# Kernel tuning notes

Hardware: AMD Instinct MI355X
Metric: run time of the kernel (lower is better)

Reference implementation:

```python
import jax, jax.numpy as jnp
import numpy as np

LATENT = 128   # latent_size
FDIM = 32      # feature_dim per plane
FSIZE = 512    # feature_size -> grid is (FSIZE+1)^2
HID = 256      # hidden_dim
N = 500000     # number of query points
IN_DIM = 3
G = FSIZE + 1
SDF_IN = 3 * FDIM + LATENT + IN_DIM  # 227


def setup_inputs() -> dict:
    key = jax.random.key(0)
    ks = jax.random.split(key, 6)
    x = jax.random.normal(ks[0], (N, LATENT + IN_DIM), jnp.float32)
    # 3 tri-planes, each [FDIM, G, G], init randn*0.01 as in FeaturePlanes
    P = jax.random.normal(ks[1], (3, FDIM, G, G), jnp.float32) * 0.01

    def lin(k, fan_in, fan_out):
        s = 1.0 / np.sqrt(fan_in)
        kw, kb = jax.random.split(k)
        W = jax.random.uniform(kw, (fan_in, fan_out), jnp.float32, -s, s)
        b = jax.random.uniform(kb, (fan_out,), jnp.float32, -s, s)
        return W, b

    W0, b0 = lin(ks[2], SDF_IN, HID)
    W1, b1 = lin(ks[3], HID, HID)
    W2, b2 = lin(ks[4], HID, 1)
    return dict(x=x, P=P, W0=W0, b0=b0, W1=W1, b1=b1, W2=W2, b2=b2)


def _sample_plane(plane, uv):
    """Bilinear grid_sample, align_corners=True, padding_mode='border'.
    plane: [C, G, G]; uv: [Npts, 2] with uv[:,0]->width(x), uv[:,1]->height(y).
    Returns [Npts, C]."""
    g = jnp.clip((uv + 1.0) * 0.5 * (G - 1), 0.0, G - 1)  # unnormalize + border clamp
    gx, gy = g[:, 0], g[:, 1]
    x0f, y0f = jnp.floor(gx), jnp.floor(gy)
    x0 = x0f.astype(jnp.int32)
    y0 = y0f.astype(jnp.int32)
    x1 = jnp.minimum(x0 + 1, G - 1)
    y1 = jnp.minimum(y0 + 1, G - 1)
    wx = gx - x0f
    wy = gy - y0f
    v00 = plane[:, y0, x0]  # [C, Npts]
    v01 = plane[:, y0, x1]
    v10 = plane[:, y1, x0]
    v11 = plane[:, y1, x1]
    top = v00 * (1.0 - wx) + v01 * wx
    bot = v10 * (1.0 - wx) + v11 * wx
    return (top * (1.0 - wy) + bot * wy).T  # [Npts, C]


def reference(x, P, W0, b0, W1, b1, W2, b2):
    in_latents = x[:, :LATENT]
    in_x = x[:, -3:]
    coords = jax.lax.stop_gradient(in_x)  # matches .detach() before grid_sample
    # dimension pairs (0,1), (0,2), (1,2) -> one bilinear lookup each, vmapped
    uv = jnp.stack([coords[:, [0, 1]], coords[:, [0, 2]], coords[:, [1, 2]]])  # [3,N,2]
    feats = jax.vmap(_sample_plane)(P, uv)              # [3, N, FDIM]
    feats = jnp.transpose(feats, (1, 0, 2)).reshape(x.shape[0], 3 * FDIM)
    net_in = jnp.concatenate([in_latents, in_x, feats], axis=-1)  # [N, 227]
    h = jax.nn.relu(net_in @ W0 + b0)
    h = jax.nn.relu(h @ W1 + b1)
    out = (h @ W2 + b2).squeeze(-1)  # [N]
    return out
```

## Files before the change

kernel.cpp:

```cpp
#include <hip/hip_runtime.h>
#include <stdint.h>

#define XDIM 131
#define GSZ 513
#define TROWS 64
#define SC_OFF 32768

typedef __attribute__((ext_vector_type(8))) short bf16x8;
typedef __attribute__((ext_vector_type(4))) float f32x4;
typedef unsigned int uint32;

__device__ __forceinline__ unsigned short f2bf(float f) {
  uint32 u = __float_as_uint(f);
  u += 0x7fffu + ((u >> 16) & 1u);
  return (unsigned short)(u >> 16);
}
__device__ __forceinline__ float bf2f(unsigned short s) {
  return __uint_as_float(((uint32)s) << 16);
}
__device__ __forceinline__ uint32 pk2bf(float a, float b) {
  return (uint32)f2bf(a) | ((uint32)f2bf(b) << 16);
}
__device__ __forceinline__ int slot16(int r) { return (r * 16) ^ (((r >> 3) & 1) << 5); }

__global__ void prep_pt(const float* __restrict__ P, unsigned short* __restrict__ Pt) {
  int i = blockIdx.x * 256 + threadIdx.x;
  const int CELLS = 3 * GSZ * GSZ;
  if (i >= CELLS) return;
  int pl = i / (GSZ * GSZ);
  int yx = i - pl * (GSZ * GSZ);
  const float* src = P + (size_t)pl * 32 * GSZ * GSZ + yx;
  const size_t GG = (size_t)GSZ * GSZ;
  uint4* dst = (uint4*)(Pt + (size_t)i * 32);
#pragma unroll
  for (int w = 0; w < 4; ++w) {
    uint4 t;
    t.x = pk2bf(src[(w * 8 + 0) * GG], src[(w * 8 + 1) * GG]);
    t.y = pk2bf(src[(w * 8 + 2) * GG], src[(w * 8 + 3) * GG]);
    t.z = pk2bf(src[(w * 8 + 4) * GG], src[(w * 8 + 5) * GG]);
    t.w = pk2bf(src[(w * 8 + 6) * GG], src[(w * 8 + 7) * GG]);
    dst[w] = t;
  }
}

__global__ void prep_w(const float* __restrict__ W0, const float* __restrict__ W1,
                       unsigned short* __restrict__ W0g, unsigned short* __restrict__ W1g) {
  int i = blockIdx.x * 256 + threadIdx.x;
  int sel = i >> 13;
  int t = i & 8191;
  int kb = t >> 10;
  int g  = (t >> 8) & 3;
  int n  = t & 255;
  float vv[8];
#pragma unroll
  for (int j = 0; j < 8; ++j) {
    int k = kb * 32 + g * 8 + j;
    float val;
    if (sel == 0) {
      int src = (k < 131) ? k : ((k >= 136 && k < 232) ? k - 5 : -1);
      val = (src >= 0) ? W0[src * 256 + n] : 0.f;
    } else {
      val = W1[k * 256 + n];
    }
    vv[j] = val;
  }
  uint4 o;
  o.x = pk2bf(vv[0], vv[1]);
  o.y = pk2bf(vv[2], vv[3]);
  o.z = pk2bf(vv[4], vv[5]);
  o.w = pk2bf(vv[6], vv[7]);
  unsigned short* dst = (sel == 0 ? W0g : W1g) + (size_t)t * 8;
  *(uint4*)dst = o;
}

__device__ __forceinline__ void gemm64(const unsigned char* __restrict__ lds,
                                       const unsigned short* __restrict__ Wg,
                                       int cg, int lr, int lg, f32x4 (&acc)[4][4])
{
  bf16x8 a[4], b[4], an[4], bn[4];
  const int aoff = lg * 1024;
  const unsigned short* wrow = Wg + ((size_t)lg * 256 + cg * 64 + lr) * 8;

#pragma unroll
  for (int mf = 0; mf < 4; ++mf)
    a[mf] = *(const bf16x8*)(lds + aoff + slot16(mf * 16 + lr));
#pragma unroll
  for (int nf = 0; nf < 4; ++nf)
    b[nf] = *(const bf16x8*)(wrow + nf * 128);

#pragma unroll
  for (int kb = 0; kb < 8; ++kb) {
    if (kb < 7) {
      const unsigned char* ab = lds + (kb + 1) * 4096 + aoff;
      const unsigned short* wr = wrow + (size_t)(kb + 1) * 8192;
#pragma unroll
      for (int mf = 0; mf < 4; ++mf)
        an[mf] = *(const bf16x8*)(ab + slot16(mf * 16 + lr));
#pragma unroll
      for (int nf = 0; nf < 4; ++nf)
        bn[nf] = *(const bf16x8*)(wr + nf * 128);
    }
#pragma unroll
    for (int nf = 0; nf < 4; ++nf)
#pragma unroll
      for (int mf = 0; mf < 4; ++mf)
        acc[mf][nf] = __builtin_amdgcn_mfma_f32_16x16x32_bf16(a[mf], b[nf], acc[mf][nf], 0, 0, 0);
#pragma unroll
    for (int i = 0; i < 4; ++i) { a[i] = an[i]; b[i] = bn[i]; }
  }
}

template<int USE_PT>
__global__ __launch_bounds__(256, 3) void sdf_tile(
    const float* __restrict__ x, const float* __restrict__ P,
    const unsigned short* __restrict__ Pt,
    const unsigned short* __restrict__ W0g, const unsigned short* __restrict__ W1g,
    const float* __restrict__ b0, const float* __restrict__ b1,
    const float* __restrict__ W2, const float* __restrict__ b2v,
    float* __restrict__ out, int Npts)
{
  __shared__ __align__(16) unsigned char lds[SC_OFF + 1024];

  const int tid = threadIdx.x;
  const int p0 = blockIdx.x * TROWS;
  const int lane = tid & 63, cg = tid >> 6;
  const int lr = lane & 15, lg = lane >> 4;

#pragma unroll
  for (int i = 0; i < 4; ++i) {
    int t = i * 256 + tid;
    int cb = t & 15, r = t >> 4;
    int p = min(p0 + r, Npts - 1);
    const float* src = x + (size_t)p * XDIM + cb * 8;
    uint4 v;
    v.x = pk2bf(src[0], src[1]);
    v.y = pk2bf(src[2], src[3]);
    v.z = pk2bf(src[4], src[5]);
    v.w = pk2bf(src[6], src[7]);
    *(uint4*)(lds + cb * 1024 + slot16(r)) = v;
  }
  if (tid < 64) {
    int p = min(p0 + tid, Npts - 1);
    const float* xr = x + (size_t)p * XDIM + 128;
    uint4 v;
    v.x = pk2bf(xr[0], xr[1]);
    v.y = pk2bf(xr[2], 0.f);
    v.z = 0u; v.w = 0u;
    *(uint4*)(lds + 16 * 1024 + slot16(tid)) = v;
  } else {
    uint4 z = {0u, 0u, 0u, 0u};
    ((uint4*)(lds + 29 * 1024))[tid - 64] = z;
  }

  {
    int p_l = tid >> 2, q = tid & 3;
    int p = min(p0 + p_l, Npts - 1);
    const float* xr = x + (size_t)p * XDIM + 128;
    float cc0 = xr[0], cc1 = xr[1], cc2 = xr[2];
#pragma unroll
    for (int pl = 0; pl < 3; ++pl) {
      float u = (pl == 2) ? cc1 : cc0;
      float v = (pl == 0) ? cc1 : cc2;
      float gx = fminf(fmaxf((u + 1.f) * 256.f, 0.f), 512.f);
      float gy = fminf(fmaxf((v + 1.f) * 256.f, 0.f), 512.f);
      float x0f = floorf(gx), y0f = floorf(gy);
      int x0 = (int)x0f, y0 = (int)y0f;
      int x1 = min(x0 + 1, GSZ - 1), y1 = min(y0 + 1, GSZ - 1);
      float wx = gx - x0f, wy = gy - y0f;
      float w00 = (1.f - wx) * (1.f - wy), w01 = wx * (1.f - wy);
      float w10 = (1.f - wx) * wy,        w11 = wx * wy;
      float f[8];
      if (USE_PT) {
        const unsigned short* pb = Pt + (size_t)pl * GSZ * GSZ * 32 + q * 8;
        bf16x8 v00 = *(const bf16x8*)(pb + (size_t)(y0 * GSZ + x0) * 32);
        bf16x8 v01 = *(const bf16x8*)(pb + (size_t)(y0 * GSZ + x1) * 32);
        bf16x8 v10 = *(const bf16x8*)(pb + (size_t)(y1 * GSZ + x0) * 32);
        bf16x8 v11 = *(const bf16x8*)(pb + (size_t)(y1 * GSZ + x1) * 32);
#pragma unroll
        for (int j = 0; j < 8; ++j) {
          f[j] = w00 * bf2f((unsigned short)v00[j]) + w01 * bf2f((unsigned short)v01[j])
               + w10 * bf2f((unsigned short)v10[j]) + w11 * bf2f((unsigned short)v11[j]);
        }
      } else {
#pragma unroll
        for (int j = 0; j < 8; ++j) {
          const float* pc = P + (size_t)(pl * 32 + q * 8 + j) * GSZ * GSZ;
          f[j] = w00 * pc[y0 * GSZ + x0] + w01 * pc[y0 * GSZ + x1]
               + w10 * pc[y1 * GSZ + x0] + w11 * pc[y1 * GSZ + x1];
        }
      }
      uint4 fv;
      fv.x = pk2bf(f[0], f[1]);
      fv.y = pk2bf(f[2], f[3]);
      fv.z = pk2bf(f[4], f[5]);
      fv.w = pk2bf(f[6], f[7]);
      *(uint4*)(lds + (17 + pl * 4 + q) * 1024 + slot16(p_l)) = fv;
    }
  }
  __syncthreads();

  {
    f32x4 acc[4][4];
#pragma unroll
    for (int mf = 0; mf < 4; ++mf)
#pragma unroll
      for (int nf = 0; nf < 4; ++nf) acc[mf][nf] = (f32x4){0.f, 0.f, 0.f, 0.f};
    gemm64(lds, W0g, cg, lr, lg, acc);
    __syncthreads();
#pragma unroll
    for (int nf = 0; nf < 4; ++nf) {
      int col = cg * 64 + nf * 16 + lr;
      float bs = b0[col];
      unsigned char* base = lds + (col >> 3) * 1024 + (col & 7) * 2;
#pragma unroll
      for (int mf = 0; mf < 4; ++mf)
#pragma unroll
        for (int reg = 0; reg < 4; ++reg) {
          int row = mf * 16 + lg * 4 + reg;
          *(unsigned short*)(base + slot16(row)) = f2bf(fmaxf(acc[mf][nf][reg] + bs, 0.f));
        }
    }
  }
  __syncthreads();

  {
    f32x4 acc[4][4];
#pragma unroll
    for (int mf = 0; mf < 4; ++mf)
#pragma unroll
      for (int nf = 0; nf < 4; ++nf) acc[mf][nf] = (f32x4){0.f, 0.f, 0.f, 0.f};
    gemm64(lds, W1g, cg, lr, lg, acc);

    float part[4][4];
#pragma unroll
    for (int mf = 0; mf < 4; ++mf)
#pragma unroll
      for (int reg = 0; reg < 4; ++reg) part[mf][reg] = 0.f;
#pragma unroll
    for (int nf = 0; nf < 4; ++nf) {
      int col = cg * 64 + nf * 16 + lr;
      float bs = b1[col];
      float w2v = W2[col];
#pragma unroll
      for (int mf = 0; mf < 4; ++mf)
#pragma unroll
        for (int reg = 0; reg < 4; ++reg)
          part[mf][reg] += fmaxf(acc[mf][nf][reg] + bs, 0.f) * w2v;
    }
#pragma unroll
    for (int mf = 0; mf < 4; ++mf)
#pragma unroll
      for (int reg = 0; reg < 4; ++reg) {
        float v = part[mf][reg];
        v += __shfl_xor(v, 1);
        v += __shfl_xor(v, 2);
        v += __shfl_xor(v, 4);
        v += __shfl_xor(v, 8);
        part[mf][reg] = v;
      }
    if (lr == 0) {
      float* sc = (float*)(lds + SC_OFF) + cg * 64;
#pragma unroll
      for (int mf = 0; mf < 4; ++mf) {
        float4 pv;
        pv.x = part[mf][0]; pv.y = part[mf][1]; pv.z = part[mf][2]; pv.w = part[mf][3];
        *(float4*)(sc + mf * 16 + lg * 4) = pv;
      }
    }
  }
  __syncthreads();
  if (tid < 64) {
    const float* sc = (const float*)(lds + SC_OFF);
    float s = sc[tid] + sc[64 + tid] + sc[128 + tid] + sc[192 + tid] + b2v[0];
    int p = p0 + tid;
    if (p < Npts) out[p] = s;
  }
}

extern "C" void kernel_launch(void* const* d_in, const int* in_sizes, int n_in,
                              void* d_out, int out_size, void* d_ws, size_t ws_size,
                              hipStream_t stream)
{
  const float* x  = (const float*)d_in[0];
  const float* P  = (const float*)d_in[1];
  const float* W0 = (const float*)d_in[2];
  const float* b0 = (const float*)d_in[3];
  const float* W1 = (const float*)d_in[4];
  const float* b1 = (const float*)d_in[5];
  const float* W2 = (const float*)d_in[6];
  const float* b2 = (const float*)d_in[7];
  float* out = (float*)d_out;
  int Npts = in_sizes[0] / XDIM;

  const size_t PT_BYTES = (size_t)3 * GSZ * GSZ * 32 * 2;
  const size_t WG_BYTES = (size_t)8192 * 8 * 2;
  char* ws = (char*)d_ws;

  int use_pt = (ws_size >= PT_BYTES + 2 * WG_BYTES) ? 1 : 0;
  unsigned short *Ptb = nullptr, *W0g, *W1g;
  if (use_pt) {
    Ptb = (unsigned short*)ws;
    W0g = (unsigned short*)(ws + PT_BYTES);
    W1g = (unsigned short*)(ws + PT_BYTES + WG_BYTES);
  } else {
    W0g = (unsigned short*)ws;
    W1g = (unsigned short*)(ws + WG_BYTES);
  }

  prep_w<<<64, 256, 0, stream>>>(W0, W1, W0g, W1g);
  if (use_pt) prep_pt<<<(3 * GSZ * GSZ + 255) / 256, 256, 0, stream>>>(P, Ptb);

  int nblk = (Npts + TROWS - 1) / TROWS;
  if (use_pt)
    sdf_tile<1><<<nblk, 256, 0, stream>>>(x, P, Ptb, W0g, W1g, b0, b1, W2, b2, out, Npts);
  else
    sdf_tile<0><<<nblk, 256, 0, stream>>>(x, P, Ptb, W0g, W1g, b0, b1, W2, b2, out, Npts);
}
```

Measured before the change: 331.2 us.

## Split bilinear gather into separate kernel and simplify MLP GEMM loop

Adds a standalone gather kernel that does all twelve tri-plane bilinear lookups per point, issuing every load before any arithmetic, and writes bf16 features to a workspace buffer. The MLP kernel then loads these features with coalesced reads instead of doing latency-bound random gathers between its GEMMs. It also raises occupancy to 4 blocks per SM, drops the GEMM register double-buffering in favour of s_setprio around the MFMA loop, and uses the hardware packed bf16 convert instruction. The cost is an extra round trip through global memory for the features, about 96 MB written and read, plus one more kernel launch. The new path runs only when the workspace is large enough.

Result: slower. 363.5 us (+9.8%).

```diff
diff --git a/kernel.cpp b/kernel.cpp
--- a/kernel.cpp
+++ b/kernel.cpp
@@ -10,16 +10,16 @@
 typedef __attribute__((ext_vector_type(4))) float f32x4;
 typedef unsigned int uint32;
 
+__device__ __forceinline__ uint32 pk2bf(float a, float b) {
+  uint32 r;
+  asm volatile("v_cvt_pk_bf16_f32 %0, %1, %2" : "=v"(r) : "v"(a), "v"(b));
+  return r;
+}
 __device__ __forceinline__ unsigned short f2bf(float f) {
-  uint32 u = __float_as_uint(f);
-  u += 0x7fffu + ((u >> 16) & 1u);
-  return (unsigned short)(u >> 16);
+  return (unsigned short)pk2bf(f, f);
 }
 __device__ __forceinline__ float bf2f(unsigned short s) {
   return __uint_as_float(((uint32)s) << 16);
-}
-__device__ __forceinline__ uint32 pk2bf(float a, float b) {
-  return (uint32)f2bf(a) | ((uint32)f2bf(b) << 16);
 }
 __device__ __forceinline__ int slot16(int r) { return (r * 16) ^ (((r >> 3) & 1) << 5); }
 
@@ -73,47 +73,89 @@
   *(uint4*)dst = o;
 }
 
-__device__ __forceinline__ void gemm64(const unsigned char* __restrict__ lds,
+__global__ __launch_bounds__(256) void k_gather(
+    const float* __restrict__ x, const unsigned short* __restrict__ Pt,
+    unsigned short* __restrict__ feats, int Npts)
+{
+  int idx = blockIdx.x * 256 + threadIdx.x;
+  int p = min(idx >> 2, Npts - 1);
+  int q = idx & 3;
+  const float* xr = x + (size_t)p * XDIM + 128;
+  float cc0 = xr[0], cc1 = xr[1], cc2 = xr[2];
+
+  const unsigned short* pp[12];
+  float w[12];
+#pragma unroll
+  for (int pl = 0; pl < 3; ++pl) {
+    float u = (pl == 2) ? cc1 : cc0;
+    float v = (pl == 0) ? cc1 : cc2;
+    float gx = fminf(fmaxf((u + 1.f) * 256.f, 0.f), 512.f);
+    float gy = fminf(fmaxf((v + 1.f) * 256.f, 0.f), 512.f);
+    float x0f = floorf(gx), y0f = floorf(gy);
+    int x0 = (int)x0f, y0 = (int)y0f;
+    int x1 = min(x0 + 1, GSZ - 1), y1 = min(y0 + 1, GSZ - 1);
+    float wx = gx - x0f, wy = gy - y0f;
+    w[pl * 4 + 0] = (1.f - wx) * (1.f - wy);
+    w[pl * 4 + 1] = wx * (1.f - wy);
+    w[pl * 4 + 2] = (1.f - wx) * wy;
+    w[pl * 4 + 3] = wx * wy;
+    const unsigned short* pb = Pt + (size_t)pl * GSZ * GSZ * 32 + q * 8;
+    pp[pl * 4 + 0] = pb + (size_t)(y0 * GSZ + x0) * 32;
+    pp[pl * 4 + 1] = pb + (size_t)(y0 * GSZ + x1) * 32;
+    pp[pl * 4 + 2] = pb + (size_t)(y1 * GSZ + x0) * 32;
+    pp[pl * 4 + 3] = pb + (size_t)(y1 * GSZ + x1) * 32;
+  }
+  bf16x8 v[12];
+#pragma unroll
+  for (int j = 0; j < 12; ++j) v[j] = *(const bf16x8*)pp[j];
+
+#pragma unroll
+  for (int pl = 0; pl < 3; ++pl) {
+    float f[8];
+#pragma unroll
+    for (int j = 0; j < 8; ++j) {
+      f[j] = w[pl * 4 + 0] * bf2f((unsigned short)v[pl * 4 + 0][j])
+           + w[pl * 4 + 1] * bf2f((unsigned short)v[pl * 4 + 1][j])
+           + w[pl * 4 + 2] * bf2f((unsigned short)v[pl * 4 + 2][j])
+           + w[pl * 4 + 3] * bf2f((unsigned short)v[pl * 4 + 3][j]);
+    }
+    uint4 fv;
+    fv.x = pk2bf(f[0], f[1]);
+    fv.y = pk2bf(f[2], f[3]);
+    fv.z = pk2bf(f[4], f[5]);
+    fv.w = pk2bf(f[6], f[7]);
+    *(uint4*)(feats + (size_t)p * 96 + pl * 32 + q * 8) = fv;
+  }
+}
+
+__device__ __forceinline__ void gemm64(const unsigned char* __restrict__ lds_,
                                        const unsigned short* __restrict__ Wg,
                                        int cg, int lr, int lg, f32x4 (&acc)[4][4])
 {
-  bf16x8 a[4], b[4], an[4], bn[4];
-  const int aoff = lg * 1024;
-  const unsigned short* wrow = Wg + ((size_t)lg * 256 + cg * 64 + lr) * 8;
-
-#pragma unroll
-  for (int mf = 0; mf < 4; ++mf)
-    a[mf] = *(const bf16x8*)(lds + aoff + slot16(mf * 16 + lr));
-#pragma unroll
-  for (int nf = 0; nf < 4; ++nf)
-    b[nf] = *(const bf16x8*)(wrow + nf * 128);
-
 #pragma unroll
   for (int kb = 0; kb < 8; ++kb) {
-    if (kb < 7) {
-      const unsigned char* ab = lds + (kb + 1) * 4096 + aoff;
-      const unsigned short* wr = wrow + (size_t)(kb + 1) * 8192;
+    bf16x8 a[4];
+    const unsigned char* ab = lds_ + (kb * 4 + lg) * 1024;
+#pragma unroll
+    for (int mf = 0; mf < 4; ++mf)
+      a[mf] = *(const bf16x8*)(ab + slot16(mf * 16 + lr));
+    const unsigned short* wb = Wg + ((size_t)(kb * 4 + lg) * 256 + cg * 64 + lr) * 8;
+    __builtin_amdgcn_s_setprio(1);
+#pragma unroll
+    for (int nf = 0; nf < 4; ++nf) {
+      bf16x8 b = *(const bf16x8*)(wb + nf * 128);
 #pragma unroll
       for (int mf = 0; mf < 4; ++mf)
-        an[mf] = *(const bf16x8*)(ab + slot16(mf * 16 + lr));
-#pragma unroll
-      for (int nf = 0; nf < 4; ++nf)
-        bn[nf] = *(const bf16x8*)(wr + nf * 128);
-    }
-#pragma unroll
-    for (int nf = 0; nf < 4; ++nf)
-#pragma unroll
-      for (int mf = 0; mf < 4; ++mf)
-        acc[mf][nf] = __builtin_amdgcn_mfma_f32_16x16x32_bf16(a[mf], b[nf], acc[mf][nf], 0, 0, 0);
-#pragma unroll
-    for (int i = 0; i < 4; ++i) { a[i] = an[i]; b[i] = bn[i]; }
-  }
-}
-
-template<int USE_PT>
-__global__ __launch_bounds__(256, 3) void sdf_tile(
+        acc[mf][nf] = __builtin_amdgcn_mfma_f32_16x16x32_bf16(a[mf], b, acc[mf][nf], 0, 0, 0);
+    }
+    __builtin_amdgcn_s_setprio(0);
+  }
+}
+
+template<int MODE>
+__global__ __launch_bounds__(256, 4) void sdf_mlp(
     const float* __restrict__ x, const float* __restrict__ P,
-    const unsigned short* __restrict__ Pt,
+    const unsigned short* __restrict__ Pt, const unsigned short* __restrict__ feats,
     const unsigned short* __restrict__ W0g, const unsigned short* __restrict__ W1g,
     const float* __restrict__ b0, const float* __restrict__ b1,
     const float* __restrict__ W2, const float* __restrict__ b2v,
@@ -152,7 +194,16 @@
     ((uint4*)(lds + 29 * 1024))[tid - 64] = z;
   }
 
-  {
+  if (MODE == 0) {
+#pragma unroll
+    for (int i = 0; i < 3; ++i) {
+      int t = i * 256 + tid;
+      int r = t & 63, j = t >> 6;
+      int p = min(p0 + r, Npts - 1);
+      uint4 fv = *(const uint4*)(feats + (size_t)p * 96 + j * 8);
+      *(uint4*)(lds + (17 + j) * 1024 + slot16(r)) = fv;
+    }
+  } else {
     int p_l = tid >> 2, q = tid & 3;
     int p = min(p0 + p_l, Npts - 1);
     const float* xr = x + (size_t)p * XDIM + 128;
@@ -170,7 +221,7 @@
       float w00 = (1.f - wx) * (1.f - wy), w01 = wx * (1.f - wy);
       float w10 = (1.f - wx) * wy,        w11 = wx * wy;
       float f[8];
-      if (USE_PT) {
+      if (MODE == 1) {
         const unsigned short* pb = Pt + (size_t)pl * GSZ * GSZ * 32 + q * 8;
         bf16x8 v00 = *(const bf16x8*)(pb + (size_t)(y0 * GSZ + x0) * 32);
         bf16x8 v01 = *(const bf16x8*)(pb + (size_t)(y0 * GSZ + x1) * 32);
@@ -294,25 +345,37 @@
 
   const size_t PT_BYTES = (size_t)3 * GSZ * GSZ * 32 * 2;
   const size_t WG_BYTES = (size_t)8192 * 8 * 2;
+  const size_t FT_BYTES = (size_t)Npts * 96 * 2;
   char* ws = (char*)d_ws;
 
-  int use_pt = (ws_size >= PT_BYTES + 2 * WG_BYTES) ? 1 : 0;
-  unsigned short *Ptb = nullptr, *W0g, *W1g;
-  if (use_pt) {
+  int mode;
+  unsigned short *Ptb = nullptr, *W0g, *W1g, *ft = nullptr;
+  if (ws_size >= PT_BYTES + 2 * WG_BYTES + FT_BYTES) {
+    mode = 0;
+    Ptb = (unsigned short*)ws;
+    W0g = (unsigned short*)(ws + PT_BYTES);
+    W1g = (unsigned short*)(ws + PT_BYTES + WG_BYTES);
+    ft  = (unsigned short*)(ws + PT_BYTES + 2 * WG_BYTES);
+  } else if (ws_size >= PT_BYTES + 2 * WG_BYTES) {
+    mode = 1;
     Ptb = (unsigned short*)ws;
     W0g = (unsigned short*)(ws + PT_BYTES);
     W1g = (unsigned short*)(ws + PT_BYTES + WG_BYTES);
   } else {
+    mode = 2;
     W0g = (unsigned short*)ws;
     W1g = (unsigned short*)(ws + WG_BYTES);
   }
 
   prep_w<<<64, 256, 0, stream>>>(W0, W1, W0g, W1g);
-  if (use_pt) prep_pt<<<(3 * GSZ * GSZ + 255) / 256, 256, 0, stream>>>(P, Ptb);
+  if (mode != 2) prep_pt<<<(3 * GSZ * GSZ + 255) / 256, 256, 0, stream>>>(P, Ptb);
+  if (mode == 0) k_gather<<<(Npts * 4 + 255) / 256, 256, 0, stream>>>(x, Ptb, ft, Npts);
 
   int nblk = (Npts + TROWS - 1) / TROWS;
-  if (use_pt)
-    sdf_tile<1><<<nblk, 256, 0, stream>>>(x, P, Ptb, W0g, W1g, b0, b1, W2, b2, out, Npts);
+  if (mode == 0)
+    sdf_mlp<0><<<nblk, 256, 0, stream>>>(x, P, Ptb, ft, W0g, W1g, b0, b1, W2, b2, out, Npts);
+  else if (mode == 1)
+    sdf_mlp<1><<<nblk, 256, 0, stream>>>(x, P, Ptb, ft, W0g, W1g, b0, b1, W2, b2, out, Npts);
   else
-    sdf_tile<0><<<nblk, 256, 0, stream>>>(x, P, Ptb, W0g, W1g, b0, b1, W2, b2, out, Npts);
-}
+    sdf_mlp<2><<<nblk, 256, 0, stream>>>(x, P, Ptb, ft, W0g, W1g, b0, b1, W2, b2, out, Npts);
+}
```
